# Optimization experiments

Hardware: AMD Instinct MI355X
Metric: run time of the kernel (lower is better)

The kernel has to match this reference:

```python
import jax, jax.numpy as jnp
import numpy as np

N_NODES = 50000
N_EDGES = 1000000
HIDDEN = 64
NUM_GRAPHS = 512
EPS = 1e-5


def _instance_norm(x, seg, num_graphs):
    # per-graph, per-channel normalization (PyG InstanceNorm, affine=False)
    ones = jnp.ones((x.shape[0], 1), x.dtype)
    cnt = jnp.clip(jax.ops.segment_sum(ones, seg, num_segments=num_graphs), 1.0)
    mean = jax.ops.segment_sum(x, seg, num_segments=num_graphs) / cnt
    xc = x - mean[seg]
    var = jax.ops.segment_sum(xc * xc, seg, num_segments=num_graphs) / cnt
    return xc * jax.lax.rsqrt(var + EPS)[seg]


def setup_inputs() -> dict:
    key = jax.random.key(0)
    ks = jax.random.split(key, 10)
    emb = jax.random.normal(ks[0], (N_NODES, HIDDEN), jnp.float32)
    edge_index = jax.random.randint(ks[1], (2, N_EDGES), 0, N_NODES, jnp.int64 if jax.config.read('jax_enable_x64') else jnp.int32)
    batch = jnp.sort(jax.random.randint(ks[2], (N_NODES,), 0, NUM_GRAPHS))
    h = HIDDEN
    # channels = [2h, 4h, h, 1]
    W1 = jax.random.normal(ks[3], (2 * h, 4 * h), jnp.float32) * 0.05
    b1 = jnp.zeros((4 * h,), jnp.float32)
    W2 = jax.random.normal(ks[4], (4 * h, h), jnp.float32) * 0.05
    b2 = jnp.zeros((h,), jnp.float32)
    W3 = jax.random.normal(ks[5], (h, 1), jnp.float32) * 0.05
    b3 = jnp.zeros((1,), jnp.float32)
    return {"emb": emb, "W1": W1, "b1": b1, "W2": W2, "b2": b2,
            "W3": W3, "b3": b3, "edge_index": edge_index, "batch": batch}


def reference(emb, W1, b1, W2, b2, W3, b3, edge_index, batch):
    col, row = edge_index[0], edge_index[1]
    f12 = jnp.concatenate([emb[col], emb[row]], axis=-1)  # [E, 2h]
    seg = batch[col]  # per-edge graph id
    x = f12 @ W1 + b1                                      # [E, 4h]
    x = jax.nn.relu(_instance_norm(x, seg, NUM_GRAPHS))
    x = x @ W2 + b2                                        # [E, h]
    x = jax.nn.relu(_instance_norm(x, seg, NUM_GRAPHS))
    return x @ W3 + b3                                     # [E, 1]
```

## Files before the change

kernel.cpp:

```cpp
#include <hip/hip_runtime.h>
#include <hip/hip_bf16.h>

#define EDGES 1000000
#define NNODES 50000
#define NG 512
#define NTILES 15625
#define NCOLB 50176

typedef __attribute__((ext_vector_type(8))) short bf16x8;
typedef __attribute__((ext_vector_type(4))) float f32x4;

__device__ __forceinline__ unsigned short f2bf(float f){
  unsigned u = __float_as_uint(f);
  u += 0x7fffu + ((u >> 16) & 1u);
  return (unsigned short)(u >> 16);
}
__device__ __forceinline__ float bf2f(unsigned short h){
  return __uint_as_float(((unsigned)h) << 16);
}
__device__ __forceinline__ unsigned pk2bf(float x, float y){
  __hip_bfloat162 h = __float22bfloat162_rn(make_float2(x, y));
  union { __hip_bfloat162 h; unsigned u; } cv; cv.h = h;
  return cv.u;
}
__device__ __forceinline__ int xcd_swizzle(int bid, int nb){
  int nb8 = nb & ~7;
  if (bid >= nb8) return bid;
  int per = nb8 >> 3;
  return (bid & 7) * per + (bid >> 3);
}

__global__ void prep_all(const float* __restrict__ emb, const float* __restrict__ W1,
                         const float* __restrict__ W2,
                         unsigned short* __restrict__ emb_bf,
                         unsigned short* __restrict__ w1tn, unsigned short* __restrict__ w2t){
  int i = blockIdx.x * 256 + threadIdx.x;
  if (i < NNODES * 64){
    emb_bf[i] = f2bf(emb[i]);
  } else {
    int j = i - NNODES * 64;
    if (j < 32768){
      int jj = j >> 6, k = j & 63;
      float v = (jj < 256) ? W1[k * 256 + jj] : W1[(k + 64) * 256 + (jj - 256)];
      w1tn[j] = f2bf(v);
    } else {
      int jj = j - 32768;
      if (jj < 16384){
        int n = jj >> 8, k = jj & 255;
        w2t[jj] = f2bf(W2[k * 64 + n]);
      }
    }
  }
}

__global__ void hists(const int* __restrict__ ei, const int* __restrict__ batch,
                      unsigned* __restrict__ hist, unsigned* __restrict__ chist){
  __shared__ unsigned h[NG];
  int t = threadIdx.x;
  h[t] = 0; h[t + 256] = 0;
  __syncthreads();
  for (int i = 0; i < 4; i++){
    int e = blockIdx.x * 1024 + i * 256 + t;
    if (e < EDGES){
      int cn = ei[e];
      atomicAdd(&chist[cn], 1u);
      atomicAdd(&h[batch[cn]], 1u);
    }
  }
  __syncthreads();
  atomicAdd(&hist[t], h[t]);
  atomicAdd(&hist[t + 256], h[t + 256]);
}

__global__ void col_scan1(const unsigned* __restrict__ chist, unsigned* __restrict__ cpre,
                          unsigned* __restrict__ bsum){
  __shared__ unsigned s[256];
  int t = threadIdx.x;
  int i = blockIdx.x * 256 + t;
  unsigned v = (i < NNODES) ? chist[i] : 0u;
  s[t] = v;
  __syncthreads();
  for (int o = 1; o < 256; o <<= 1){
    unsigned u = (t >= o) ? s[t - o] : 0u;
    __syncthreads();
    s[t] += u;
    __syncthreads();
  }
  cpre[i] = s[t] - v;
  if (t == 255) bsum[blockIdx.x] = s[255];
}

__global__ void col_scan2(unsigned* __restrict__ bsum){
  __shared__ unsigned s[256];
  int t = threadIdx.x;
  unsigned v = (t < 196) ? bsum[t] : 0u;
  s[t] = v;
  __syncthreads();
  for (int o = 1; o < 256; o <<= 1){
    unsigned u = (t >= o) ? s[t - o] : 0u;
    __syncthreads();
    s[t] += u;
    __syncthreads();
  }
  if (t < 196) bsum[t] = s[t] - v;
}

__global__ void col_scan3(unsigned* __restrict__ cpre, const unsigned* __restrict__ bsum){
  int i = blockIdx.x * 256 + threadIdx.x;
  cpre[i] += bsum[blockIdx.x];
}

__global__ void col_scatter(const int* __restrict__ ei, const int* __restrict__ batch,
                            unsigned* __restrict__ cpre, int4* __restrict__ emeta){
  for (int i = 0; i < 4; i++){
    int e = blockIdx.x * 1024 + i * 256 + threadIdx.x;
    if (e < EDGES){
      int cn = ei[e];
      int pos = (int)atomicAdd(&cpre[cn], 1u);
      emeta[pos] = make_int4(cn, ei[EDGES + e], batch[cn], e);
    }
  }
}

__global__ __launch_bounds__(256) void node_gemm(
    const unsigned short* __restrict__ emb_bf, const unsigned short* __restrict__ w1tn,
    unsigned short* __restrict__ P)
{
  __shared__ unsigned short As[64 * 72];
  int t = threadIdx.x;
  int n0 = blockIdx.x * 64;
  {
    int nl = t >> 2, part = t & 3;
    int node = n0 + nl; if (node >= NNODES) node = 0;
    const int4* src = (const int4*)(emb_bf + node * 64 + part * 16);
    int4* dst = (int4*)(As + nl * 72 + part * 16);
    dst[0] = src[0]; dst[1] = src[1];
  }
  __syncthreads();
  int w = t >> 6, lane = t & 63, q = lane >> 4, c = lane & 15;
  f32x4 acc[4][8];
  for (int a = 0; a < 4; a++) for (int b = 0; b < 8; b++) for (int r = 0; r < 4; r++) acc[a][b][r] = 0.f;
  for (int k0 = 0; k0 < 64; k0 += 32){
    bf16x8 af[4];
    for (int tt = 0; tt < 4; tt++) af[tt] = *(const bf16x8*)(As + (tt * 16 + c) * 72 + k0 + q * 8);
    for (int n4 = 0; n4 < 8; n4++){
      bf16x8 bw = *(const bf16x8*)(w1tn + (w * 128 + n4 * 16 + c) * 64 + k0 + q * 8);
      for (int tt = 0; tt < 4; tt++)
        acc[tt][n4] = __builtin_amdgcn_mfma_f32_16x16x32_bf16(af[tt], bw, acc[tt][n4], 0, 0, 0);
    }
  }
  for (int tt = 0; tt < 4; tt++){
    for (int r = 0; r < 4; r++){
      int node = n0 + tt * 16 + q * 4 + r;
      if (node < NNODES){
        unsigned short* dst = P + (size_t)node * 512 + w * 128 + c;
        for (int n4 = 0; n4 < 8; n4++) dst[n4 * 16] = f2bf(acc[tt][n4][r]);
      }
    }
  }
}

__global__ __launch_bounds__(256) void k1_gather(
    const unsigned short* __restrict__ P, const int4* __restrict__ emeta,
    float* __restrict__ sum1, float* __restrict__ sqs1)
{
  int lane = threadIdx.x & 63;
  int bid = xcd_swizzle(blockIdx.x, gridDim.x);
  int wid = (bid * 256 + threadIdx.x) >> 6;
  if (wid >= NTILES) return;
  int p0 = wid * 64;
  int4 me = emeta[p0 + lane];
  int c4 = lane * 4;
  int s0 = __builtin_amdgcn_readlane(me.z, 0);
  bool uni = (__ballot(me.z == s0) == ~0ull);
  float sm0 = 0.f, sm1 = 0.f, sm2 = 0.f, sm3 = 0.f;
  float q0 = 0.f, q1 = 0.f, q2 = 0.f, q3 = 0.f;
  if (uni){
    int cprev = __builtin_amdgcn_readlane(me.x, 0);
    ushort4 a = *(const ushort4*)(P + (size_t)cprev * 512 + c4);
    ushort4 cur[4];
    #pragma unroll
    for (int j = 0; j < 4; j++){
      int re = __builtin_amdgcn_readlane(me.y, j);
      cur[j] = *(const ushort4*)(P + (size_t)re * 512 + 256 + c4);
    }
    for (int eb = 0; eb < 64; eb += 4){
      ushort4 nxt[4];
      if (eb < 60){
        #pragma unroll
        for (int j = 0; j < 4; j++){
          int re = __builtin_amdgcn_readlane(me.y, eb + 4 + j);
          nxt[j] = *(const ushort4*)(P + (size_t)re * 512 + 256 + c4);
        }
      }
      #pragma unroll
      for (int j = 0; j < 4; j++){
        int ce = __builtin_amdgcn_readlane(me.x, eb + j);
        if (ce != cprev){ a = *(const ushort4*)(P + (size_t)ce * 512 + c4); cprev = ce; }
        float x0 = bf2f(a.x) + bf2f(cur[j].x);
        float x1 = bf2f(a.y) + bf2f(cur[j].y);
        float x2v = bf2f(a.z) + bf2f(cur[j].z);
        float x3 = bf2f(a.w) + bf2f(cur[j].w);
        sm0 += x0; q0 += x0 * x0;
        sm1 += x1; q1 += x1 * x1;
        sm2 += x2v; q2 += x2v * x2v;
        sm3 += x3; q3 += x3 * x3;
      }
      #pragma unroll
      for (int j = 0; j < 4; j++) cur[j] = nxt[j];
    }
    float* sp = sum1 + s0 * 256 + c4;
    float* qp = sqs1 + s0 * 256 + c4;
    atomicAdd(sp + 0, sm0); atomicAdd(sp + 1, sm1); atomicAdd(sp + 2, sm2); atomicAdd(sp + 3, sm3);
    atomicAdd(qp + 0, q0);  atomicAdd(qp + 1, q1);  atomicAdd(qp + 2, q2);  atomicAdd(qp + 3, q3);
  } else {
    int cur = s0;
    int cprev = -1;
    ushort4 a = make_ushort4(0,0,0,0);
    for (int e = 0; e < 64; e++){
      int ce = __builtin_amdgcn_readlane(me.x, e);
      int re = __builtin_amdgcn_readlane(me.y, e);
      if (ce != cprev){ a = *(const ushort4*)(P + (size_t)ce * 512 + c4); cprev = ce; }
      ushort4 b = *(const ushort4*)(P + (size_t)re * 512 + 256 + c4);
      int s = __builtin_amdgcn_readlane(me.z, e);
      if (s != cur){
        float* sp = sum1 + cur * 256 + c4;
        float* qp = sqs1 + cur * 256 + c4;
        atomicAdd(sp + 0, sm0); atomicAdd(sp + 1, sm1); atomicAdd(sp + 2, sm2); atomicAdd(sp + 3, sm3);
        atomicAdd(qp + 0, q0);  atomicAdd(qp + 1, q1);  atomicAdd(qp + 2, q2);  atomicAdd(qp + 3, q3);
        sm0 = sm1 = sm2 = sm3 = 0.f; q0 = q1 = q2 = q3 = 0.f;
        cur = s;
      }
      float x0 = bf2f(a.x) + bf2f(b.x);
      float x1 = bf2f(a.y) + bf2f(b.y);
      float x2v = bf2f(a.z) + bf2f(b.z);
      float x3 = bf2f(a.w) + bf2f(b.w);
      sm0 += x0; q0 += x0 * x0;
      sm1 += x1; q1 += x1 * x1;
      sm2 += x2v; q2 += x2v * x2v;
      sm3 += x3; q3 += x3 * x3;
    }
    float* sp = sum1 + cur * 256 + c4;
    float* qp = sqs1 + cur * 256 + c4;
    atomicAdd(sp + 0, sm0); atomicAdd(sp + 1, sm1); atomicAdd(sp + 2, sm2); atomicAdd(sp + 3, sm3);
    atomicAdd(qp + 0, q0);  atomicAdd(qp + 1, q1);  atomicAdd(qp + 2, q2);  atomicAdd(qp + 3, q3);
  }
}

__global__ void finalize1(const float* __restrict__ sum1, const float* __restrict__ sqs1,
                          const unsigned* __restrict__ hist, float* __restrict__ r1,
                          float* __restrict__ mr1){
  int i = blockIdx.x * 256 + threadIdx.x;
  int g = i >> 8;
  float cnt = fmaxf((float)hist[g], 1.f);
  float m = sum1[i] / cnt;
  float v = sqs1[i] / cnt - m * m;
  v = fmaxf(v, 0.f);
  float r = rsqrtf(v + 1e-5f);
  r1[i] = r;
  mr1[i] = m * r;
}

__global__ void finalize2(const float* __restrict__ sum2, const float* __restrict__ sqs2,
                          const unsigned* __restrict__ hist, float* __restrict__ r2,
                          float* __restrict__ mr2){
  int i = blockIdx.x * 256 + threadIdx.x;
  int g = i >> 6;
  float cnt = fmaxf((float)hist[g], 1.f);
  float m = sum2[i] / cnt;
  float v = sqs2[i] / cnt - m * m;
  v = fmaxf(v, 0.f);
  float r = rsqrtf(v + 1e-5f);
  r2[i] = r;
  mr2[i] = m * r;
}

__global__ __launch_bounds__(256) void k2_fused(
    const unsigned short* __restrict__ P, const unsigned short* __restrict__ w2t,
    const int4* __restrict__ emeta,
    const float* __restrict__ r1, const float* __restrict__ mr1,
    float* __restrict__ sum2, float* __restrict__ sqs2,
    unsigned short* __restrict__ x2t)
{
  __shared__ unsigned short Y[64 * 264];
  __shared__ int segl[64];
  __shared__ short rsegA[64];
  __shared__ unsigned char rloA[65];
  __shared__ int nrunS;
  int t = threadIdx.x;
  int bid = xcd_swizzle(blockIdx.x, gridDim.x);
  int p0 = bid * 64;
  int w = t >> 6, lane = t & 63, q = lane >> 4, c = lane & 15;
  int c4 = lane * 4;
  int elb0 = w * 16;
  int4 me = emeta[p0 + elb0 + (lane & 15)];

  ushort4 bb[16];
  #pragma unroll
  for (int e = 0; e < 16; e++){
    int re = __builtin_amdgcn_readlane(me.y, e);
    bb[e] = *(const ushort4*)(P + (size_t)re * 512 + 256 + c4);
  }
  int cprev = __builtin_amdgcn_readlane(me.x, 0);
  ushort4 a = *(const ushort4*)(P + (size_t)cprev * 512 + c4);
  int s0g = __builtin_amdgcn_readlane(me.z, 0);
  float4 r4  = *(const float4*)(r1  + s0g * 256 + c4);
  float4 mr4 = *(const float4*)(mr1 + s0g * 256 + c4);

  if (t < 64) segl[t] = emeta[p0 + t].z;
  if (w == 0){
    int sN = segl[lane];
    int nxt = (lane < 63) ? segl[lane + 1] : sN;
    unsigned long long mask = __ballot(sN != nxt);
    if (lane == 0){
      if (mask == 0ull){
        nrunS = 1; rloA[0] = 0; rloA[1] = 64; rsegA[0] = (short)sN;
      } else {
        int n = 0, cur = segl[0];
        rsegA[0] = (short)cur; rloA[0] = 0;
        for (int i = 1; i < 64; i++)
          if (segl[i] != cur){ cur = segl[i]; n++; rsegA[n] = (short)cur; rloA[n] = (unsigned char)i; }
        rloA[n + 1] = 64; nrunS = n + 1;
      }
    }
  }
  __syncthreads();
  int nrun = nrunS;
  bool uni = (nrun == 1);

  #pragma unroll
  for (int e = 0; e < 16; e++){
    int ce = __builtin_amdgcn_readlane(me.x, e);
    if (ce != cprev){ a = *(const ushort4*)(P + (size_t)ce * 512 + c4); cprev = ce; }
    float4 rr4 = r4, mm4 = mr4;
    if (!uni){
      int s = __builtin_amdgcn_readlane(me.z, e);
      rr4 = *(const float4*)(r1  + s * 256 + c4);
      mm4 = *(const float4*)(mr1 + s * 256 + c4);
    }
    float y0 = fmaxf(0.f, (bf2f(a.x) + bf2f(bb[e].x)) * rr4.x - mm4.x);
    float y1 = fmaxf(0.f, (bf2f(a.y) + bf2f(bb[e].y)) * rr4.y - mm4.y);
    float y2 = fmaxf(0.f, (bf2f(a.z) + bf2f(bb[e].z)) * rr4.z - mm4.z);
    float y3 = fmaxf(0.f, (bf2f(a.w) + bf2f(bb[e].w)) * rr4.w - mm4.w);
    uint2 pk;
    pk.x = pk2bf(y0, y1);
    pk.y = pk2bf(y2, y3);
    *(uint2*)(Y + (elb0 + e) * 264 + c4) = pk;
  }
  __syncthreads();

  f32x4 acc2[4];
  for (int tt = 0; tt < 4; tt++) for (int r = 0; r < 4; r++) acc2[tt][r] = 0.f;
  int ch2 = w * 16 + c;
  for (int kc = 0; kc < 8; kc++){
    int k0 = kc * 32;
    bf16x8 bfr = *(const bf16x8*)(w2t + ch2 * 256 + k0 + q * 8);
    for (int tt = 0; tt < 4; tt++){
      bf16x8 afr = *(const bf16x8*)(Y + (tt * 16 + c) * 264 + k0 + q * 8);
      acc2[tt] = __builtin_amdgcn_mfma_f32_16x16x32_bf16(afr, bfr, acc2[tt], 0, 0, 0);
    }
  }

  if (uni){
    int s = segl[0];
    float sm = 0.f, sq = 0.f;
    for (int tt = 0; tt < 4; tt++)
      for (int r = 0; r < 4; r++){
        float v = acc2[tt][r];
        sm += v; sq += v * v;
      }
    sm += __shfl_xor(sm, 16); sq += __shfl_xor(sq, 16);
    sm += __shfl_xor(sm, 32); sq += __shfl_xor(sq, 32);
    if (q == 0){
      atomicAdd(&sum2[s * 64 + ch2], sm);
      atomicAdd(&sqs2[s * 64 + ch2], sq);
    }
  } else {
    for (int rr = 0; rr < nrun; rr++){
      int s = rsegA[rr], lo = rloA[rr], hi = rloA[rr + 1];
      float sm = 0.f, sq = 0.f;
      for (int tt = 0; tt < 4; tt++){
        int elb = tt * 16 + q * 4;
        for (int r = 0; r < 4; r++){
          int el = elb + r;
          if (el >= lo && el < hi){
            float v = acc2[tt][r];
            sm += v; sq += v * v;
          }
        }
      }
      sm += __shfl_xor(sm, 16); sq += __shfl_xor(sq, 16);
      sm += __shfl_xor(sm, 32); sq += __shfl_xor(sq, 32);
      if (q == 0){
        atomicAdd(&sum2[s * 64 + ch2], sm);
        atomicAdd(&sqs2[s * 64 + ch2], sq);
      }
    }
  }
  for (int tt = 0; tt < 4; tt++){
    uint2 pk;
    pk.x = pk2bf(acc2[tt][0], acc2[tt][1]);
    pk.y = pk2bf(acc2[tt][2], acc2[tt][3]);
    *(uint2*)(x2t + (size_t)ch2 * EDGES + p0 + tt * 16 + q * 4) = pk;
  }
}

__global__ __launch_bounds__(256) void k3_out(
    const unsigned short* __restrict__ x2t, const int4* __restrict__ emeta,
    const float* __restrict__ r2, const float* __restrict__ mr2,
    const float* __restrict__ W3, const float* __restrict__ b3, float* __restrict__ out)
{
  int pp4 = (blockIdx.x * 256 + threadIdx.x) * 4;
  if (pp4 >= EDGES) return;
  int4 m0 = emeta[pp4 + 0];
  int4 m1 = emeta[pp4 + 1];
  int4 m2 = emeta[pp4 + 2];
  int4 m3 = emeta[pp4 + 3];
  float a0 = 0.f, a1 = 0.f, a2 = 0.f, a3 = 0.f;
  if (m0.z == m3.z && m0.z == m1.z && m0.z == m2.z){
    const float* rp = r2  + m0.z * 64;
    const float* mp = mr2 + m0.z * 64;
    #pragma unroll 8
    for (int ch = 0; ch < 64; ch++){
      ushort4 v = *(const ushort4*)(x2t + (size_t)ch * EDGES + pp4);
      float rr = rp[ch], mm = mp[ch], wv = W3[ch];
      a0 += fmaxf(0.f, bf2f(v.x) * rr - mm) * wv;
      a1 += fmaxf(0.f, bf2f(v.y) * rr - mm) * wv;
      a2 += fmaxf(0.f, bf2f(v.z) * rr - mm) * wv;
      a3 += fmaxf(0.f, bf2f(v.w) * rr - mm) * wv;
    }
  } else {
    #pragma unroll 8
    for (int ch = 0; ch < 64; ch++){
      ushort4 v = *(const ushort4*)(x2t + (size_t)ch * EDGES + pp4);
      float wv = W3[ch];
      a0 += fmaxf(0.f, bf2f(v.x) * r2[m0.z * 64 + ch] - mr2[m0.z * 64 + ch]) * wv;
      a1 += fmaxf(0.f, bf2f(v.y) * r2[m1.z * 64 + ch] - mr2[m1.z * 64 + ch]) * wv;
      a2 += fmaxf(0.f, bf2f(v.z) * r2[m2.z * 64 + ch] - mr2[m2.z * 64 + ch]) * wv;
      a3 += fmaxf(0.f, bf2f(v.w) * r2[m3.z * 64 + ch] - mr2[m3.z * 64 + ch]) * wv;
    }
  }
  float bv = b3[0];
  out[m0.w] = a0 + bv;
  out[m1.w] = a1 + bv;
  out[m2.w] = a2 + bv;
  out[m3.w] = a3 + bv;
}

extern "C" void kernel_launch(void* const* d_in, const int* in_sizes, int n_in,
                              void* d_out, int out_size, void* d_ws, size_t ws_size,
                              hipStream_t stream)
{
  (void)in_sizes; (void)n_in; (void)out_size;
  const float* emb = (const float*)d_in[0];
  const float* W1  = (const float*)d_in[1];
  const float* W2  = (const float*)d_in[3];
  const float* W3  = (const float*)d_in[5];
  const float* b3  = (const float*)d_in[6];
  const int* ei    = (const int*)d_in[7];
  const int* batch = (const int*)d_in[8];
  float* out = (float*)d_out;

  char* p = (char*)d_ws;
  size_t off = 0;
  auto take = [&](size_t n) -> char* {
    char* r = p + off;
    off += (n + 255) & ~(size_t)255;
    return r;
  };

  unsigned short* emb_bf = (unsigned short*)take((size_t)NNODES * 64 * 2);
  unsigned short* w1tn   = (unsigned short*)take(32768 * 2);
  unsigned short* w2t    = (unsigned short*)take(16384 * 2);
  int4* emeta = (int4*)take((size_t)EDGES * 16);
  unsigned short* P   = (unsigned short*)take((size_t)NNODES * 512 * 2);
  unsigned short* x2t = (unsigned short*)take((size_t)EDGES * 64 * 2);
  float* r1  = (float*)take(512 * 256 * 4);
  float* mr1 = (float*)take(512 * 256 * 4);
  float* r2  = (float*)take(512 * 64 * 4);
  float* mr2 = (float*)take(512 * 64 * 4);
  unsigned* cpre = (unsigned*)take(NCOLB * 4);
  unsigned* bsum = (unsigned*)take(256 * 4);
  char* zbase = p + off;
  unsigned* hist  = (unsigned*)take(NG * 4);
  unsigned* chist = (unsigned*)take(NCOLB * 4);
  float* sum1 = (float*)take(512 * 256 * 4);
  float* sqs1 = (float*)take(512 * 256 * 4);
  float* sum2 = (float*)take(512 * 64 * 4);
  float* sqs2 = (float*)take(512 * 64 * 4);
  size_t zsize = (size_t)((p + off) - zbase);

  if (ws_size < off) return;

  hipMemsetAsync(zbase, 0, zsize, stream);
  prep_all<<<12692, 256, 0, stream>>>(emb, W1, W2, emb_bf, w1tn, w2t);
  hists<<<977, 256, 0, stream>>>(ei, batch, hist, chist);
  col_scan1<<<196, 256, 0, stream>>>(chist, cpre, bsum);
  col_scan2<<<1, 256, 0, stream>>>(bsum);
  col_scan3<<<196, 256, 0, stream>>>(cpre, bsum);
  col_scatter<<<977, 256, 0, stream>>>(ei, batch, cpre, emeta);
  node_gemm<<<(NNODES + 63) / 64, 256, 0, stream>>>(emb_bf, w1tn, P);
  k1_gather<<<(NTILES + 3) / 4, 256, 0, stream>>>(P, emeta, sum1, sqs1);
  finalize1<<<512, 256, 0, stream>>>(sum1, sqs1, hist, r1, mr1);
  k2_fused<<<NTILES, 256, 0, stream>>>(P, w2t, emeta, r1, mr1, sum2, sqs2, x2t);
  finalize2<<<128, 256, 0, stream>>>(sum2, sqs2, hist, r2, mr2);
  k3_out<<<977, 256, 0, stream>>>(x2t, emeta, r2, mr2, W3, b3, out);
}
```

Measured before the change: 583.8 us.

## Process two tiles per wave with triple-buffered gathers and LDS-staged segment atomics

k1_gather now has each wave handle two consecutive 64-edge tiles and keeps running sums across them while the segment id stays the same. Partial sums for the block's first and last segments go through LDS atomics before a single global atomic per channel, which cuts global atomic traffic. The uniform path now loads both the col and row rows with a 3-deep prefetch ring instead of reusing the col row, which issues more loads but gives more memory-level parallelism. Launch bounds add an occupancy hint and the grid is halved.

```diff
diff --git a/kernel.cpp b/kernel.cpp
--- a/kernel.cpp
+++ b/kernel.cpp
@@ -160,90 +160,123 @@
   }
 }
 
-__global__ __launch_bounds__(256) void k1_gather(
+__global__ __launch_bounds__(256, 5) void k1_gather(
     const unsigned short* __restrict__ P, const int4* __restrict__ emeta,
     float* __restrict__ sum1, float* __restrict__ sqs1)
 {
-  int lane = threadIdx.x & 63;
+  __shared__ float ls[1024];
+  int t = threadIdx.x;
   int bid = xcd_swizzle(blockIdx.x, gridDim.x);
-  int wid = (bid * 256 + threadIdx.x) >> 6;
-  if (wid >= NTILES) return;
-  int p0 = wid * 64;
-  int4 me = emeta[p0 + lane];
-  int c4 = lane * 4;
-  int s0 = __builtin_amdgcn_readlane(me.z, 0);
-  bool uni = (__ballot(me.z == s0) == ~0ull);
+  int tile0 = bid * 8;
+  for (int i = t; i < 1024; i += 256) ls[i] = 0.f;
+  int s0 = emeta[tile0 * 64].z;
+  int elast = tile0 * 64 + 511; if (elast >= EDGES) elast = EDGES - 1;
+  int s1 = emeta[elast].z;
+  __syncthreads();
+
+  int w = t >> 6, lane = t & 63, c4 = lane * 4;
+
   float sm0 = 0.f, sm1 = 0.f, sm2 = 0.f, sm3 = 0.f;
   float q0 = 0.f, q1 = 0.f, q2 = 0.f, q3 = 0.f;
-  if (uni){
-    int cprev = __builtin_amdgcn_readlane(me.x, 0);
-    ushort4 a = *(const ushort4*)(P + (size_t)cprev * 512 + c4);
-    ushort4 cur[4];
-    #pragma unroll
-    for (int j = 0; j < 4; j++){
-      int re = __builtin_amdgcn_readlane(me.y, j);
-      cur[j] = *(const ushort4*)(P + (size_t)re * 512 + 256 + c4);
-    }
-    for (int eb = 0; eb < 64; eb += 4){
-      ushort4 nxt[4];
-      if (eb < 60){
+  int curs = -1;
+
+  auto FLUSH = [&](int s){
+    if (s == s0 || s == s1){
+      float* base = ls + ((s == s0) ? 0 : 512) + c4;
+      atomicAdd(base + 0, sm0); atomicAdd(base + 1, sm1);
+      atomicAdd(base + 2, sm2); atomicAdd(base + 3, sm3);
+      atomicAdd(base + 256, q0); atomicAdd(base + 257, q1);
+      atomicAdd(base + 258, q2); atomicAdd(base + 259, q3);
+    } else {
+      float* sp = sum1 + s * 256 + c4;
+      float* qp = sqs1 + s * 256 + c4;
+      atomicAdd(sp + 0, sm0); atomicAdd(sp + 1, sm1); atomicAdd(sp + 2, sm2); atomicAdd(sp + 3, sm3);
+      atomicAdd(qp + 0, q0);  atomicAdd(qp + 1, q1);  atomicAdd(qp + 2, q2);  atomicAdd(qp + 3, q3);
+    }
+    sm0 = sm1 = sm2 = sm3 = 0.f; q0 = q1 = q2 = q3 = 0.f;
+  };
+
+  for (int ti = 0; ti < 2; ti++){
+    int tile = tile0 + w * 2 + ti;
+    if (tile >= NTILES) continue;
+    int4 me = emeta[tile * 64 + lane];
+    int sseg = __builtin_amdgcn_readlane(me.z, 0);
+    bool uni = (__ballot(me.z == sseg) == ~0ull);
+    if (uni){
+      if (sseg != curs){
+        if (curs >= 0) FLUSH(curs);
+        curs = sseg;
+      }
+      ushort4 rv[3][4], cv[3][4];
+      #pragma unroll
+      for (int g = 0; g < 2; g++){
         #pragma unroll
         for (int j = 0; j < 4; j++){
-          int re = __builtin_amdgcn_readlane(me.y, eb + 4 + j);
-          nxt[j] = *(const ushort4*)(P + (size_t)re * 512 + 256 + c4);
+          int e = g * 4 + j;
+          int re = __builtin_amdgcn_readlane(me.y, e);
+          int ce = __builtin_amdgcn_readlane(me.x, e);
+          rv[g][j] = *(const ushort4*)(P + (size_t)re * 512 + 256 + c4);
+          cv[g][j] = *(const ushort4*)(P + (size_t)ce * 512 + c4);
         }
       }
       #pragma unroll
-      for (int j = 0; j < 4; j++){
-        int ce = __builtin_amdgcn_readlane(me.x, eb + j);
+      for (int g = 0; g < 16; g++){
+        if (g < 14){
+          int bn = (g + 2) % 3;
+          #pragma unroll
+          for (int j = 0; j < 4; j++){
+            int e = (g + 2) * 4 + j;
+            int re = __builtin_amdgcn_readlane(me.y, e);
+            int ce = __builtin_amdgcn_readlane(me.x, e);
+            rv[bn][j] = *(const ushort4*)(P + (size_t)re * 512 + 256 + c4);
+            cv[bn][j] = *(const ushort4*)(P + (size_t)ce * 512 + c4);
+          }
+        }
+        int b = g % 3;
+        #pragma unroll
+        for (int j = 0; j < 4; j++){
+          float x0 = bf2f(cv[b][j].x) + bf2f(rv[b][j].x);
+          float x1 = bf2f(cv[b][j].y) + bf2f(rv[b][j].y);
+          float x2v = bf2f(cv[b][j].z) + bf2f(rv[b][j].z);
+          float x3 = bf2f(cv[b][j].w) + bf2f(rv[b][j].w);
+          sm0 += x0; q0 += x0 * x0;
+          sm1 += x1; q1 += x1 * x1;
+          sm2 += x2v; q2 += x2v * x2v;
+          sm3 += x3; q3 += x3 * x3;
+        }
+      }
+    } else {
+      int cprev = -1;
+      ushort4 a = make_ushort4(0, 0, 0, 0);
+      for (int e = 0; e < 64; e++){
+        int ce = __builtin_amdgcn_readlane(me.x, e);
+        int re = __builtin_amdgcn_readlane(me.y, e);
+        int s = __builtin_amdgcn_readlane(me.z, e);
+        if (s != curs){
+          if (curs >= 0) FLUSH(curs);
+          curs = s;
+        }
         if (ce != cprev){ a = *(const ushort4*)(P + (size_t)ce * 512 + c4); cprev = ce; }
-        float x0 = bf2f(a.x) + bf2f(cur[j].x);
-        float x1 = bf2f(a.y) + bf2f(cur[j].y);
-        float x2v = bf2f(a.z) + bf2f(cur[j].z);
-        float x3 = bf2f(a.w) + bf2f(cur[j].w);
+        ushort4 b = *(const ushort4*)(P + (size_t)re * 512 + 256 + c4);
+        float x0 = bf2f(a.x) + bf2f(b.x);
+        float x1 = bf2f(a.y) + bf2f(b.y);
+        float x2v = bf2f(a.z) + bf2f(b.z);
+        float x3 = bf2f(a.w) + bf2f(b.w);
         sm0 += x0; q0 += x0 * x0;
         sm1 += x1; q1 += x1 * x1;
         sm2 += x2v; q2 += x2v * x2v;
         sm3 += x3; q3 += x3 * x3;
       }
-      #pragma unroll
-      for (int j = 0; j < 4; j++) cur[j] = nxt[j];
-    }
-    float* sp = sum1 + s0 * 256 + c4;
-    float* qp = sqs1 + s0 * 256 + c4;
-    atomicAdd(sp + 0, sm0); atomicAdd(sp + 1, sm1); atomicAdd(sp + 2, sm2); atomicAdd(sp + 3, sm3);
-    atomicAdd(qp + 0, q0);  atomicAdd(qp + 1, q1);  atomicAdd(qp + 2, q2);  atomicAdd(qp + 3, q3);
-  } else {
-    int cur = s0;
-    int cprev = -1;
-    ushort4 a = make_ushort4(0,0,0,0);
-    for (int e = 0; e < 64; e++){
-      int ce = __builtin_amdgcn_readlane(me.x, e);
-      int re = __builtin_amdgcn_readlane(me.y, e);
-      if (ce != cprev){ a = *(const ushort4*)(P + (size_t)ce * 512 + c4); cprev = ce; }
-      ushort4 b = *(const ushort4*)(P + (size_t)re * 512 + 256 + c4);
-      int s = __builtin_amdgcn_readlane(me.z, e);
-      if (s != cur){
-        float* sp = sum1 + cur * 256 + c4;
-        float* qp = sqs1 + cur * 256 + c4;
-        atomicAdd(sp + 0, sm0); atomicAdd(sp + 1, sm1); atomicAdd(sp + 2, sm2); atomicAdd(sp + 3, sm3);
-        atomicAdd(qp + 0, q0);  atomicAdd(qp + 1, q1);  atomicAdd(qp + 2, q2);  atomicAdd(qp + 3, q3);
-        sm0 = sm1 = sm2 = sm3 = 0.f; q0 = q1 = q2 = q3 = 0.f;
-        cur = s;
-      }
-      float x0 = bf2f(a.x) + bf2f(b.x);
-      float x1 = bf2f(a.y) + bf2f(b.y);
-      float x2v = bf2f(a.z) + bf2f(b.z);
-      float x3 = bf2f(a.w) + bf2f(b.w);
-      sm0 += x0; q0 += x0 * x0;
-      sm1 += x1; q1 += x1 * x1;
-      sm2 += x2v; q2 += x2v * x2v;
-      sm3 += x3; q3 += x3 * x3;
-    }
-    float* sp = sum1 + cur * 256 + c4;
-    float* qp = sqs1 + cur * 256 + c4;
-    atomicAdd(sp + 0, sm0); atomicAdd(sp + 1, sm1); atomicAdd(sp + 2, sm2); atomicAdd(sp + 3, sm3);
-    atomicAdd(qp + 0, q0);  atomicAdd(qp + 1, q1);  atomicAdd(qp + 2, q2);  atomicAdd(qp + 3, q3);
+    }
+  }
+  if (curs >= 0) FLUSH(curs);
+
+  __syncthreads();
+  atomicAdd(&sum1[s0 * 256 + t], ls[t]);
+  atomicAdd(&sqs1[s0 * 256 + t], ls[256 + t]);
+  if (s1 != s0){
+    atomicAdd(&sum1[s1 * 256 + t], ls[512 + t]);
+    atomicAdd(&sqs1[s1 * 256 + t], ls[768 + t]);
   }
 }
 
@@ -500,7 +533,7 @@
   col_scan3<<<196, 256, 0, stream>>>(cpre, bsum);
   col_scatter<<<977, 256, 0, stream>>>(ei, batch, cpre, emeta);
   node_gemm<<<(NNODES + 63) / 64, 256, 0, stream>>>(emb_bf, w1tn, P);
-  k1_gather<<<(NTILES + 3) / 4, 256, 0, stream>>>(P, emeta, sum1, sqs1);
+  k1_gather<<<(NTILES + 7) / 8, 256, 0, stream>>>(P, emeta, sum1, sqs1);
   finalize1<<<512, 256, 0, stream>>>(sum1, sqs1, hist, r1, mr1);
   k2_fused<<<NTILES, 256, 0, stream>>>(P, w2t, emeta, r1, mr1, sum2, sqs2, x2t);
   finalize2<<<128, 256, 0, stream>>>(sum2, sqs2, hist, r2, mr2);
```

Result: faster. 509.8 us (-12.7%).
